# Performance work log

Hardware: AMD Instinct MI355X
Metric: run time of the kernel (lower is better)

Reference implementation:

```python
import jax, jax.numpy as jnp
import numpy as np

B, H, S, D = 2, 16, 2048, 64
NUM_BUCKETS = 32
MAX_DISTANCE = 256


def setup_inputs() -> dict:
    key = jax.random.key(0)
    kq, kk, kv, kb, kl = jax.random.split(key, 5)
    q = jax.random.normal(kq, (B, H, S, D), dtype=jnp.float32)
    k = jax.random.normal(kk, (B, H, S, D), dtype=jnp.float32)
    v = jax.random.normal(kv, (B, H, S, D), dtype=jnp.float32)
    bias_table = jax.random.normal(kb, (NUM_BUCKETS, H), dtype=jnp.float32)
    event_length = jax.random.randint(kl, (B,), 1, S + 1, dtype=jnp.int64)
    return {"q": q, "k": k, "v": v, "bias_table": bias_table, "event_length": event_length}


def _relative_position_bucket(relative_position):
    # T5-style bucketing exactly as the torch module: n = -rel_pos
    half = NUM_BUCKETS // 2  # 16
    n = -relative_position
    is_small = n < half
    # guard log for the branch not taken (n<=0); where() masks it out
    nf = jnp.maximum(n, 1).astype(jnp.float32)
    val_if_large = half + jnp.minimum(
        jnp.log(nf / half) / np.log(MAX_DISTANCE / half) * (NUM_BUCKETS - half),
        NUM_BUCKETS - 1 - half,
    ).astype(jnp.int32)
    ret = jnp.where(is_small, n, val_if_large)
    return jnp.clip(ret, 0, NUM_BUCKETS - 1)


def _compute_bias(bias_table, seq_len):
    ctx = jnp.arange(seq_len)[:, None]
    mem = jnp.arange(seq_len)[None, :]
    rp_bucket = _relative_position_bucket(mem - ctx)  # (S,S)
    values = bias_table[rp_bucket]                    # (S,S,H)
    return jnp.transpose(values, (2, 0, 1))[None]     # (1,H,S,S)


def reference(q, k, v, bias_table, event_length):
    seq_len = q.shape[2]
    head_dim = q.shape[3]
    # scaled QK^T: (B,H,S,S)
    logits = jnp.einsum("bhsd,bhtd->bhst", q, k) / np.sqrt(head_dim).astype(np.float32)
    logits = logits + _compute_bias(bias_table, seq_len)
    # key-side padding mask from per-event lengths
    mask = jnp.arange(seq_len)[None, None, None, :] < event_length[:, None, None, None]
    logits = jnp.where(mask, logits, jnp.float32(-1e9))
    attn = jax.nn.softmax(logits, axis=-1)
    # dropout p=0.01 omitted (eval-mode deterministic reference)
    return jnp.einsum("bhst,bhtd->bhsd", attn, v)
```

## Files before the change

### kernel.cpp

```cpp
#include <hip/hip_runtime.h>

#define B_ 2
#define H_ 16
#define S_ 2048
#define D_ 64
#define BQ 128
#define BK 64
#define NQB (S_ / BQ)
#define LDSTR 72
#define LOG2E 1.4426950408889634f
#define FIXM 10.0f

#if __has_builtin(__builtin_amdgcn_exp2f)
#define EXP2F(x) __builtin_amdgcn_exp2f(x)
#else
#define EXP2F(x) __expf((x) * 0.6931471805599453f)
#endif

typedef _Float16 half8 __attribute__((ext_vector_type(8)));
typedef _Float16 half4 __attribute__((ext_vector_type(4)));
typedef __fp16   fp16x2 __attribute__((ext_vector_type(2)));
typedef float floatx4 __attribute__((ext_vector_type(4)));

typedef _Float16 KlArr[BK][LDSTR];
typedef _Float16 VtArr[D_][LDSTR];

#define VT_OFF  18432
#define LUT_OFF 36864
#define OX_STR  66
#define LX_OFF  33792

__global__ __launch_bounds__(512, 4)
void t5_attn_kernel(const float* __restrict__ qg_, const float* __restrict__ kg_,
                    const float* __restrict__ vg_, const float* __restrict__ bt,
                    const int* __restrict__ elen, float* __restrict__ outg_)
{
    __shared__ __align__(16) unsigned char smem[37888];
    KlArr* Kl  = reinterpret_cast<KlArr*>(smem);
    VtArr* Vt  = reinterpret_cast<VtArr*>(smem + VT_OFF);
    float* lut = reinterpret_cast<float*>(smem + LUT_OFF);

    const int tid  = threadIdx.x;
    const int wave = tid >> 6;
    const int lane = tid & 63;
    const int quad = lane >> 4;
    const int t16  = lane & 15;
    const int wq   = wave >> 1;
    const int kh   = wave & 1;

    const int f    = blockIdx.x + NQB * (blockIdx.y + H_ * blockIdx.z);
    const int qblk = (f >> 3) & 15;
    const int bh   = (f & 7) | ((f >> 7) << 3);
    const int h    = bh & 15;
    const int b    = bh >> 4;

    if (tid < 256) {
        int n = tid;
        int bucket;
        if (n < 16) {
            bucket = n;
        } else {
            int vl = (int)(__log2f((float)n * 0.0625f) * 4.0f);
            bucket = 16 + (vl < 15 ? vl : 15);
        }
        lut[n] = bt[bucket * H_ + h] * LOG2E - FIXM;
    }
    const float sh_next = FIXM - bt[h] * LOG2E;
    const float sh_far  = FIXM - bt[31 * H_ + h] * LOG2E;

    const int len = (elen[1] == 0) ? elen[2 * b] : elen[b];
    const int ntiles = (len + BK - 1) >> 6;

    const size_t bhoff = ((size_t)b * H_ + h) * (size_t)(S_ * D_);
    const float* qptr = qg_ + bhoff;
    const float* kptr = kg_ + bhoff;
    const float* vptr = vg_ + bhoff;
    float*       optr = outg_ + bhoff;

    half8 qf[2][2];
    {
        const float qscale = 0.125f * LOG2E;
        #pragma unroll
        for (int rg = 0; rg < 2; ++rg) {
            const int row = qblk * BQ + wq * 32 + rg * 16 + t16;
            const float* qp = qptr + (size_t)row * D_ + quad * 8;
            #pragma unroll
            for (int c = 0; c < 2; ++c) {
                const float4* pq = reinterpret_cast<const float4*>(qp + c * 32);
                float4 x0 = pq[0], x1 = pq[1];
                half8 hv;
                hv[0] = (_Float16)(x0.x * qscale); hv[1] = (_Float16)(x0.y * qscale);
                hv[2] = (_Float16)(x0.z * qscale); hv[3] = (_Float16)(x0.w * qscale);
                hv[4] = (_Float16)(x1.x * qscale); hv[5] = (_Float16)(x1.y * qscale);
                hv[6] = (_Float16)(x1.z * qscale); hv[7] = (_Float16)(x1.w * qscale);
                qf[rg][c] = hv;
            }
        }
    }

    floatx4 zero4 = {0.f, 0.f, 0.f, 0.f};
    floatx4 acc[2][4];
    float l_[2];
    #pragma unroll
    for (int rg = 0; rg < 2; ++rg) {
        #pragma unroll
        for (int nb = 0; nb < 4; ++nb) acc[rg][nb] = zero4;
        l_[rg] = 0.f;
    }

    const int i_lo = qblk * BQ + wq * 32;

    auto pack4 = [](const floatx4& v) -> half4 {
        fp16x2 lo = __builtin_amdgcn_cvt_pkrtz(v[0], v[1]);
        fp16x2 hi = __builtin_amdgcn_cvt_pkrtz(v[2], v[3]);
        half4 w;
        w[0] = (_Float16)lo[0]; w[1] = (_Float16)lo[1];
        w[2] = (_Float16)hi[0]; w[3] = (_Float16)hi[1];
        return w;
    };

    float4 kx[2];
    float  vx[8];
    auto prefetch = [&](int kt) {
        const int row = tid >> 3;
        const int c8  = (tid & 7) << 3;
        const float4* pp = reinterpret_cast<const float4*>(
            kptr + ((size_t)(kt * BK + row) * D_ + c8));
        kx[0] = pp[0];
        kx[1] = pp[1];
        const int key8 = kt * BK + wave * 8;
        #pragma unroll
        for (int jj = 0; jj < 8; ++jj)
            vx[jj] = vptr[(size_t)(key8 + jj) * D_ + lane];
    };
    auto stage = [&](int buf) {
        const int row = tid >> 3;
        const int c8  = (tid & 7) << 3;
        half8 hv;
        hv[0]=(_Float16)kx[0].x; hv[1]=(_Float16)kx[0].y; hv[2]=(_Float16)kx[0].z; hv[3]=(_Float16)kx[0].w;
        hv[4]=(_Float16)kx[1].x; hv[5]=(_Float16)kx[1].y; hv[6]=(_Float16)kx[1].z; hv[7]=(_Float16)kx[1].w;
        *reinterpret_cast<half8*>(&Kl[buf][row][c8]) = hv;
        half8 vv;
        #pragma unroll
        for (int jj = 0; jj < 8; ++jj) vv[jj] = (_Float16)vx[jj];
        *reinterpret_cast<half8*>(&Vt[buf][lane][wave * 8]) = vv;
    };

    prefetch(0);
    stage(0);
    __syncthreads();

    for (int kt = 0; kt < ntiles; ++kt) {
        const int cur = kt & 1;
        const bool more = (kt + 1) < ntiles;
        if (more) prefetch(kt + 1);

        const int keybase = kt * BK + kh * 32;

        floatx4 sa[2][2];
        #pragma unroll
        for (int rg = 0; rg < 2; ++rg)
            #pragma unroll
            for (int nb = 0; nb < 2; ++nb) sa[rg][nb] = zero4;
        __builtin_amdgcn_s_setprio(1);
        #pragma unroll
        for (int kc = 0; kc < 2; ++kc) {
            #pragma unroll
            for (int nb = 0; nb < 2; ++nb) {
                half8 af = *reinterpret_cast<const half8*>(
                    &Kl[cur][kh * 32 + nb * 16 + t16][kc * 32 + quad * 8]);
                sa[0][nb] = __builtin_amdgcn_mfma_f32_16x16x32_f16(af, qf[0][kc], sa[0][nb], 0, 0, 0);
                sa[1][nb] = __builtin_amdgcn_mfma_f32_16x16x32_f16(af, qf[1][kc], sa[1][nb], 0, 0, 0);
            }
        }
        __builtin_amdgcn_s_setprio(0);

        if (i_lo + 31 <= keybase) {
            #pragma unroll
            for (int rg = 0; rg < 2; ++rg)
                #pragma unroll
                for (int nb = 0; nb < 2; ++nb)
                    #pragma unroll
                    for (int r = 0; r < 4; ++r) sa[rg][nb][r] -= sh_next;
        } else if (i_lo >= keybase + 247) {
            #pragma unroll
            for (int rg = 0; rg < 2; ++rg)
                #pragma unroll
                for (int nb = 0; nb < 2; ++nb)
                    #pragma unroll
                    for (int r = 0; r < 4; ++r) sa[rg][nb][r] -= sh_far;
        } else {
            #pragma unroll
            for (int rg = 0; rg < 2; ++rg) {
                const int d0 = i_lo + rg * 16 + t16 - keybase - quad * 4;
                #pragma unroll
                for (int nb = 0; nb < 2; ++nb) {
                    #pragma unroll
                    for (int r = 0; r < 4; ++r) {
                        int d = d0 - nb * 16 - r;
                        d = d < 0 ? 0 : (d > 255 ? 255 : d);
                        sa[rg][nb][r] += lut[d];
                    }
                }
            }
        }
        if ((kt == ntiles - 1) && (len & 63)) {
            #pragma unroll
            for (int nb = 0; nb < 2; ++nb) {
                #pragma unroll
                for (int r = 0; r < 4; ++r) {
                    bool valid = (keybase + nb * 16 + quad * 4 + r) < len;
                    #pragma unroll
                    for (int rg = 0; rg < 2; ++rg)
                        sa[rg][nb][r] = valid ? sa[rg][nb][r] : -1e30f;
                }
            }
        }

        #pragma unroll
        for (int rg = 0; rg < 2; ++rg) {
            float ssum = 0.f;
            #pragma unroll
            for (int nb = 0; nb < 2; ++nb)
                #pragma unroll
                for (int r = 0; r < 4; ++r) {
                    sa[rg][nb][r] = EXP2F(sa[rg][nb][r]);
                    ssum += sa[rg][nb][r];
                }
            l_[rg] += ssum;
        }

        {
            half4 aA0 = pack4(sa[0][0]);
            half4 aB0 = pack4(sa[0][1]);
            half4 aA1 = pack4(sa[1][0]);
            half4 aB1 = pack4(sa[1][1]);
            __builtin_amdgcn_s_setprio(1);
            #pragma unroll
            for (int nb = 0; nb < 4; ++nb) {
                half4 bv0 = *reinterpret_cast<const half4*>(
                    &Vt[cur][nb * 16 + t16][kh * 32 + quad * 4]);
                half4 bv1 = *reinterpret_cast<const half4*>(
                    &Vt[cur][nb * 16 + t16][kh * 32 + 16 + quad * 4]);
                acc[0][nb] = __builtin_amdgcn_mfma_f32_16x16x16f16(aA0, bv0, acc[0][nb], 0, 0, 0);
                acc[0][nb] = __builtin_amdgcn_mfma_f32_16x16x16f16(aB0, bv1, acc[0][nb], 0, 0, 0);
                acc[1][nb] = __builtin_amdgcn_mfma_f32_16x16x16f16(aA1, bv0, acc[1][nb], 0, 0, 0);
                acc[1][nb] = __builtin_amdgcn_mfma_f32_16x16x16f16(aB1, bv1, acc[1][nb], 0, 0, 0);
            }
            __builtin_amdgcn_s_setprio(0);
        }

        if (more) stage(cur ^ 1);
        __syncthreads();
    }

    float lh[2];
    #pragma unroll
    for (int rg = 0; rg < 2; ++rg) {
        float lv = l_[rg];
        lv += __shfl_xor(lv, 16, 64);
        lv += __shfl_xor(lv, 32, 64);
        lh[rg] = lv;
    }
    float* Ox = reinterpret_cast<float*>(smem);
    float* Lx = reinterpret_cast<float*>(smem + LX_OFF);
    if (kh == 1) {
        #pragma unroll
        for (int rg = 0; rg < 2; ++rg) {
            #pragma unroll
            for (int nb = 0; nb < 4; ++nb)
                #pragma unroll
                for (int r = 0; r < 4; ++r)
                    Ox[(wq * 32 + rg * 16 + quad * 4 + r) * OX_STR + nb * 16 + t16] =
                        acc[rg][nb][r];
            if (quad == 0) Lx[wq * 32 + rg * 16 + t16] = lh[rg];
        }
    }
    __syncthreads();
    if (kh == 0) {
        #pragma unroll
        for (int rg = 0; rg < 2; ++rg) {
            const float inv = 1.f / (lh[rg] + Lx[wq * 32 + rg * 16 + t16]);
            #pragma unroll
            for (int r = 0; r < 4; ++r) {
                const int rowloc = quad * 4 + r;
                const float invr = __shfl(inv, (lane & 48) | rowloc, 64);
                const int row = qblk * BQ + wq * 32 + rg * 16 + rowloc;
                #pragma unroll
                for (int nb = 0; nb < 4; ++nb)
                    optr[(size_t)row * D_ + nb * 16 + t16] =
                        (acc[rg][nb][r] +
                         Ox[(wq * 32 + rg * 16 + rowloc) * OX_STR + nb * 16 + t16]) * invr;
            }
        }
    }
}

extern "C" void kernel_launch(void* const* d_in, const int* in_sizes, int n_in,
                              void* d_out, int out_size, void* d_ws, size_t ws_size,
                              hipStream_t stream) {
    const float* q  = (const float*)d_in[0];
    const float* k  = (const float*)d_in[1];
    const float* v  = (const float*)d_in[2];
    const float* bt = (const float*)d_in[3];
    const int*   el = (const int*)d_in[4];
    float* out = (float*)d_out;
    dim3 grid(NQB, H_, B_);
    t5_attn_kernel<<<grid, 512, 0, stream>>>(q, k, v, bt, el, out);
}
```

Before: 122.0 us.

## Swizzle K/V LDS tiles, fold uniform bias into MFMA init, hoist V reads

Replaces the padded LDS rows (stride 72) with unpadded rows of 64 halves and an XOR swizzle of the 8-element chunks, which shrinks shared memory and aims to avoid bank conflicts. For tiles outside the bias window, the uniform bias shift is folded into the initial accumulator of the QK MFMA, so the separate subtract pass is gone. V fragments are now read from LDS before the softmax so their latency can overlap with the exp work. Global pointers advance incrementally instead of being recomputed each tile. The risks are higher register pressure from holding the V fragments, and correctness depends on the swizzle index math matching between writes and reads.

```diff
diff --git a/kernel.cpp b/kernel.cpp
--- a/kernel.cpp
+++ b/kernel.cpp
@@ -7,7 +7,7 @@
 #define BQ 128
 #define BK 64
 #define NQB (S_ / BQ)
-#define LDSTR 72
+#define LDSH 64
 #define LOG2E 1.4426950408889634f
 #define FIXM 10.0f
 
@@ -22,29 +22,28 @@
 typedef __fp16   fp16x2 __attribute__((ext_vector_type(2)));
 typedef float floatx4 __attribute__((ext_vector_type(4)));
 
-typedef _Float16 KlArr[BK][LDSTR];
-typedef _Float16 VtArr[D_][LDSTR];
-
-#define VT_OFF  18432
-#define LUT_OFF 36864
+#define VT_OFF  16384
+#define LUT_OFF 32768
 #define OX_STR  66
 #define LX_OFF  33792
+#define SMEM_BYTES 34304
 
 __global__ __launch_bounds__(512, 4)
 void t5_attn_kernel(const float* __restrict__ qg_, const float* __restrict__ kg_,
                     const float* __restrict__ vg_, const float* __restrict__ bt,
                     const int* __restrict__ elen, float* __restrict__ outg_)
 {
-    __shared__ __align__(16) unsigned char smem[37888];
-    KlArr* Kl  = reinterpret_cast<KlArr*>(smem);
-    VtArr* Vt  = reinterpret_cast<VtArr*>(smem + VT_OFF);
-    float* lut = reinterpret_cast<float*>(smem + LUT_OFF);
+    __shared__ __align__(16) unsigned char smem[SMEM_BYTES];
+    _Float16* KL = reinterpret_cast<_Float16*>(smem);
+    _Float16* VT = reinterpret_cast<_Float16*>(smem + VT_OFF);
+    float*   lut = reinterpret_cast<float*>(smem + LUT_OFF);
 
     const int tid  = threadIdx.x;
     const int wave = tid >> 6;
     const int lane = tid & 63;
     const int quad = lane >> 4;
     const int t16  = lane & 15;
+    const int t8   = t16 & 7;
     const int wq   = wave >> 1;
     const int kh   = wave & 1;
 
@@ -119,77 +118,83 @@
         return w;
     };
 
-    float4 kx[2];
+    const int krow = tid >> 3;
+    const int kst  = krow * LDSH + (((tid & 7) ^ (krow & 7)) << 3);
+    const int vst  = lane * LDSH + ((wave ^ (lane & 7)) << 3);
+    const float* kb = kptr + (size_t)krow * D_ + ((tid & 7) << 3);
+    const float* vb = vptr + (size_t)(wave * 8) * D_ + lane;
+
+    float4 kx0, kx1;
     float  vx[8];
-    auto prefetch = [&](int kt) {
-        const int row = tid >> 3;
-        const int c8  = (tid & 7) << 3;
-        const float4* pp = reinterpret_cast<const float4*>(
-            kptr + ((size_t)(kt * BK + row) * D_ + c8));
-        kx[0] = pp[0];
-        kx[1] = pp[1];
-        const int key8 = kt * BK + wave * 8;
+    auto prefetch = [&]() {
+        const float4* pp = reinterpret_cast<const float4*>(kb);
+        kx0 = pp[0];
+        kx1 = pp[1];
+        kb += BK * D_;
         #pragma unroll
         for (int jj = 0; jj < 8; ++jj)
-            vx[jj] = vptr[(size_t)(key8 + jj) * D_ + lane];
+            vx[jj] = vb[jj * D_];
+        vb += (size_t)BK * D_;
     };
     auto stage = [&](int buf) {
-        const int row = tid >> 3;
-        const int c8  = (tid & 7) << 3;
         half8 hv;
-        hv[0]=(_Float16)kx[0].x; hv[1]=(_Float16)kx[0].y; hv[2]=(_Float16)kx[0].z; hv[3]=(_Float16)kx[0].w;
-        hv[4]=(_Float16)kx[1].x; hv[5]=(_Float16)kx[1].y; hv[6]=(_Float16)kx[1].z; hv[7]=(_Float16)kx[1].w;
-        *reinterpret_cast<half8*>(&Kl[buf][row][c8]) = hv;
+        hv[0]=(_Float16)kx0.x; hv[1]=(_Float16)kx0.y; hv[2]=(_Float16)kx0.z; hv[3]=(_Float16)kx0.w;
+        hv[4]=(_Float16)kx1.x; hv[5]=(_Float16)kx1.y; hv[6]=(_Float16)kx1.z; hv[7]=(_Float16)kx1.w;
+        *reinterpret_cast<half8*>(KL + buf * 4096 + kst) = hv;
         half8 vv;
         #pragma unroll
         for (int jj = 0; jj < 8; ++jj) vv[jj] = (_Float16)vx[jj];
-        *reinterpret_cast<half8*>(&Vt[buf][lane][wave * 8]) = vv;
+        *reinterpret_cast<half8*>(VT + buf * 4096 + vst) = vv;
     };
 
-    prefetch(0);
+    prefetch();
     stage(0);
     __syncthreads();
 
     for (int kt = 0; kt < ntiles; ++kt) {
         const int cur = kt & 1;
         const bool more = (kt + 1) < ntiles;
-        if (more) prefetch(kt + 1);
+        if (more) prefetch();
 
         const int keybase = kt * BK + kh * 32;
 
+        const bool unif_next = (i_lo + 31 <= keybase);
+        const bool unif_far  = (i_lo >= keybase + 247);
+        const float cinit = unif_next ? -sh_next : (unif_far ? -sh_far : 0.f);
+        floatx4 ci = {cinit, cinit, cinit, cinit};
+
         floatx4 sa[2][2];
         #pragma unroll
         for (int rg = 0; rg < 2; ++rg)
             #pragma unroll
-            for (int nb = 0; nb < 2; ++nb) sa[rg][nb] = zero4;
+            for (int nb = 0; nb < 2; ++nb) sa[rg][nb] = ci;
         __builtin_amdgcn_s_setprio(1);
         #pragma unroll
         for (int kc = 0; kc < 2; ++kc) {
             #pragma unroll
             for (int nb = 0; nb < 2; ++nb) {
                 half8 af = *reinterpret_cast<const half8*>(
-                    &Kl[cur][kh * 32 + nb * 16 + t16][kc * 32 + quad * 8]);
+                    KL + cur * 4096 + (kh * 32 + nb * 16 + t16) * LDSH +
+                    ((((kc << 2) | quad) ^ t8) << 3));
                 sa[0][nb] = __builtin_amdgcn_mfma_f32_16x16x32_f16(af, qf[0][kc], sa[0][nb], 0, 0, 0);
                 sa[1][nb] = __builtin_amdgcn_mfma_f32_16x16x32_f16(af, qf[1][kc], sa[1][nb], 0, 0, 0);
             }
         }
         __builtin_amdgcn_s_setprio(0);
 
-        if (i_lo + 31 <= keybase) {
-            #pragma unroll
-            for (int rg = 0; rg < 2; ++rg)
-                #pragma unroll
-                for (int nb = 0; nb < 2; ++nb)
-                    #pragma unroll
-                    for (int r = 0; r < 4; ++r) sa[rg][nb][r] -= sh_next;
-        } else if (i_lo >= keybase + 247) {
-            #pragma unroll
-            for (int rg = 0; rg < 2; ++rg)
-                #pragma unroll
-                for (int nb = 0; nb < 2; ++nb)
-                    #pragma unroll
-                    for (int r = 0; r < 4; ++r) sa[rg][nb][r] -= sh_far;
-        } else {
+        half4 bvv[4][2];
+        #pragma unroll
+        for (int nb = 0; nb < 4; ++nb) {
+            #pragma unroll
+            for (int s = 0; s < 2; ++s) {
+                bvv[nb][s] = *reinterpret_cast<const half4*>(
+                    VT + cur * 4096 + (nb * 16 + t16) * LDSH +
+                    ((((kh << 2) | (s << 1) | (quad >> 1)) ^ t8) << 3) +
+                    ((quad & 1) << 2));
+            }
+        }
+
+        if (!unif_next && !unif_far) {
             #pragma unroll
             for (int rg = 0; rg < 2; ++rg) {
                 const int d0 = i_lo + rg * 16 + t16 - keybase - quad * 4;
@@ -238,14 +243,10 @@
             __builtin_amdgcn_s_setprio(1);
             #pragma unroll
             for (int nb = 0; nb < 4; ++nb) {
-                half4 bv0 = *reinterpret_cast<const half4*>(
-                    &Vt[cur][nb * 16 + t16][kh * 32 + quad * 4]);
-                half4 bv1 = *reinterpret_cast<const half4*>(
-                    &Vt[cur][nb * 16 + t16][kh * 32 + 16 + quad * 4]);
-                acc[0][nb] = __builtin_amdgcn_mfma_f32_16x16x16f16(aA0, bv0, acc[0][nb], 0, 0, 0);
-                acc[0][nb] = __builtin_amdgcn_mfma_f32_16x16x16f16(aB0, bv1, acc[0][nb], 0, 0, 0);
-                acc[1][nb] = __builtin_amdgcn_mfma_f32_16x16x16f16(aA1, bv0, acc[1][nb], 0, 0, 0);
-                acc[1][nb] = __builtin_amdgcn_mfma_f32_16x16x16f16(aB1, bv1, acc[1][nb], 0, 0, 0);
+                acc[0][nb] = __builtin_amdgcn_mfma_f32_16x16x16f16(aA0, bvv[nb][0], acc[0][nb], 0, 0, 0);
+                acc[0][nb] = __builtin_amdgcn_mfma_f32_16x16x16f16(aB0, bvv[nb][1], acc[0][nb], 0, 0, 0);
+                acc[1][nb] = __builtin_amdgcn_mfma_f32_16x16x16f16(aA1, bvv[nb][0], acc[1][nb], 0, 0, 0);
+                acc[1][nb] = __builtin_amdgcn_mfma_f32_16x16x16f16(aB1, bvv[nb][1], acc[1][nb], 0, 0, 0);
             }
             __builtin_amdgcn_s_setprio(0);
         }
```

After: 123.5 us. Within noise of the previous version (+1.2%).
